# Kernel tuning notes

Hardware: AMD Instinct MI355X
Metric: run time of the kernel (lower is better)

Reference implementation:

```python
import jax, jax.numpy as jnp
import numpy as np

WS = 7        # window size
NH = 8        # num heads


def setup_inputs() -> dict:
    key = jax.random.key(0)
    ks = jax.random.split(key, 5)
    B, N, C = 32, 3136, 512
    x = jax.random.normal(ks[0], (B, N, C), dtype=jnp.float32)
    s = 1.0 / np.sqrt(C)
    w_qkv = jax.random.normal(ks[1], (C, 3 * C), dtype=jnp.float32) * s
    b_qkv = jax.random.normal(ks[2], (3 * C,), dtype=jnp.float32) * 0.01
    w_proj = jax.random.normal(ks[3], (C, C), dtype=jnp.float32) * s
    b_proj = jax.random.normal(ks[4], (C,), dtype=jnp.float32) * 0.01
    return {"x": x, "w_qkv": w_qkv, "b_qkv": b_qkv, "w_proj": w_proj, "b_proj": b_proj}


def reference(x, w_qkv, b_qkv, w_proj, b_proj):
    B, N, C = x.shape
    H = W = int(round(N ** 0.5))
    hd = C // NH
    t = WS * WS  # 49 tokens per window
    # window partition: (B,N,C) -> (nW, 49, C)
    xw = x.reshape(B, H // WS, WS, W // WS, WS, C)
    xw = jnp.transpose(xw, (0, 1, 3, 2, 4, 5)).reshape(-1, t, C)
    # qkv projection; NOTE: no head permute (faithful to source), so
    # q,k,v : (nW, 49, NH, hd)
    qkv = (xw @ w_qkv + b_qkv).reshape(-1, t, 3, NH, hd)
    q, k, v = qkv[:, :, 0], qkv[:, :, 1], qkv[:, :, 2]
    # q @ k^T contracts head_dim, attends over heads axis: (nW, 49, NH, NH)
    attn = jnp.einsum('wthd,wtgd->wthg', q, k) * (hd ** -0.5)
    attn = jax.nn.softmax(attn, axis=-1)
    out = jnp.einsum('wthg,wtgd->wthd', attn, v)          # (nW, 49, NH, hd)
    # faithful transpose(1,2).reshape(-1, 49, C) (scrambles layout, as in torch)
    out = jnp.transpose(out, (0, 2, 1, 3)).reshape(-1, t, C)
    out = out @ w_proj + b_proj
    # window merge back to (B, N, C)
    out = out.reshape(B, H // WS, W // WS, WS, WS, C)
    out = jnp.transpose(out, (0, 1, 3, 2, 4, 5)).reshape(B, N, C)
    return out
```

## Files before the change

kernel.cpp:

```cpp
#include <hip/hip_runtime.h>
#include <stdint.h>
#include <stddef.h>

typedef short s16;
typedef __attribute__((ext_vector_type(8))) short short8;
typedef __attribute__((ext_vector_type(4))) float floatx4;

__device__ __forceinline__ float bf2f(short s) {
    union { float f; uint32_t u; } c; c.u = ((uint32_t)(uint16_t)s) << 16; return c.f;
}
__device__ __forceinline__ short f2bf(float f) {
    union { float f; uint32_t u; } c; c.f = f;
    uint32_t u = c.u;
    u += 0x7fffu + ((u >> 16) & 1u);
    return (short)(u >> 16);
}

__global__ __launch_bounds__(256) void cvt_kernel(const float* __restrict__ src,
                                                  s16* __restrict__ dst) {
    size_t i = (size_t)blockIdx.x * 256 + threadIdx.x;
    const floatx4* s4 = (const floatx4*)src;
    floatx4 a = s4[i * 2], b = s4[i * 2 + 1];
    short8 o;
    o[0] = f2bf(a[0]); o[1] = f2bf(a[1]); o[2] = f2bf(a[2]); o[3] = f2bf(a[3]);
    o[4] = f2bf(b[0]); o[5] = f2bf(b[1]); o[6] = f2bf(b[2]); o[7] = f2bf(b[3]);
    ((short8*)dst)[i] = o;
}

__global__ __launch_bounds__(256) void transpose_kernel(const float* __restrict__ w,
                                                        s16* __restrict__ wt,
                                                        int K, int N) {
    int idx = blockIdx.x * 256 + threadIdx.x;
    if (idx >= K * N) return;
    int n = idx / K, k = idx - n * K;
    wt[idx] = f2bf(w[(size_t)k * N + n]);
}

__device__ __forceinline__ const s16* x_row_ptr(const s16* xb, int m) {
    int win = m / 49, t = m - win * 49;
    int b = win >> 6, rem = win & 63, hb = rem >> 3, wb = rem & 7;
    int r = t / 7, c = t - r * 7;
    int n = (hb * 7 + r) * 56 + wb * 7 + c;
    return xb + ((size_t)b * 3136 + n) * 512;
}

template <int MODE>
__global__ __launch_bounds__(512, 2) void gemm_kernel(const s16* __restrict__ A,
                                                      const s16* __restrict__ Bt,
                                                      const float* __restrict__ bias,
                                                      void* __restrict__ outp) {
    constexpr int NT  = (MODE == 0) ? 6 : 2;
    constexpr int CPX = (MODE == 0) ? 294 : 98;

    const int o  = (blockIdx.x & 7) * CPX + (blockIdx.x >> 3);
    const int tm = o / NT, tn = o - tm * NT;

    const int tid = threadIdx.x, wave = tid >> 6, lane = tid & 63;

    __shared__ s16 lA[3][256 * 32];
    __shared__ s16 lB[3][256 * 32];

    const int rloc = wave * 16 + (lane >> 2);
    const int gran = (lane & 3) * 8;
    const s16* a_src[2];
    const s16* b_src[2];
#pragma unroll
    for (int i = 0; i < 2; ++i) {
        int row = i * 128 + rloc;
        if (MODE == 0) a_src[i] = x_row_ptr(A, tm * 256 + row) + gran;
        else           a_src[i] = A + (size_t)(tm * 256 + row) * 512 + gran;
        b_src[i] = Bt + (size_t)(tn * 256 + row) * 512 + gran;
    }

#define STAGE_A(buf, i)                                                         \
    do {                                                                        \
        __builtin_amdgcn_global_load_lds(                                       \
            (const __attribute__((address_space(1))) void*)a_src[i],            \
            (__attribute__((address_space(3))) void*)&lA[buf][(i) * 4096 + wave * 512], \
            16, 0, 0);                                                          \
        a_src[i] += 32;                                                         \
    } while (0)
#define STAGE_B(buf, i)                                                         \
    do {                                                                        \
        __builtin_amdgcn_global_load_lds(                                       \
            (const __attribute__((address_space(1))) void*)b_src[i],            \
            (__attribute__((address_space(3))) void*)&lB[buf][(i) * 4096 + wave * 512], \
            16, 0, 0);                                                          \
        b_src[i] += 32;                                                         \
    } while (0)

    floatx4 acc[8][4];
#pragma unroll
    for (int mt = 0; mt < 8; ++mt)
#pragma unroll
        for (int nt = 0; nt < 4; ++nt)
            acc[mt][nt] = (floatx4){0.f, 0.f, 0.f, 0.f};

    const int wm = wave & 1, wn = wave >> 1;
    const int lm = lane & 15, quad = lane >> 4;
    const int koff = quad * 8;

    STAGE_A(0, 0); STAGE_A(0, 1); STAGE_B(0, 0); STAGE_B(0, 1);
    STAGE_A(1, 0); STAGE_A(1, 1); STAGE_B(1, 0); STAGE_B(1, 1);
    asm volatile("s_waitcnt vmcnt(4)" ::: "memory");
    __builtin_amdgcn_s_barrier();
    __builtin_amdgcn_sched_barrier(0);

#pragma unroll
    for (int kt = 0; kt < 16; ++kt) {
        const int cur = kt % 3, nxt = (kt + 2) % 3;
        short8 bq[4];
#pragma unroll
        for (int p = 0; p < 4; ++p) {
            if (p == 0) {
#pragma unroll
                for (int nt = 0; nt < 4; ++nt)
                    bq[nt] = *(const short8*)&lB[cur][(wn * 64 + nt * 16 + lm) * 32 + koff];
            }
            short8 a0 = *(const short8*)&lA[cur][(wm * 128 + (2 * p) * 16 + lm) * 32 + koff];
            short8 a1 = *(const short8*)&lA[cur][(wm * 128 + (2 * p + 1) * 16 + lm) * 32 + koff];

            if (kt < 14) {
                if      (p == 0) STAGE_A(nxt, 0);
                else if (p == 1) STAGE_A(nxt, 1);
                else if (p == 2) STAGE_B(nxt, 0);
                else             STAGE_B(nxt, 1);
            }

            __builtin_amdgcn_s_barrier();
            asm volatile("s_waitcnt lgkmcnt(0)" ::: "memory");
            __builtin_amdgcn_sched_barrier(0);

            __builtin_amdgcn_s_setprio(1);
#pragma unroll
            for (int nt = 0; nt < 4; ++nt)
                acc[2 * p][nt] = __builtin_amdgcn_mfma_f32_16x16x32_bf16(
                    a0, bq[nt], acc[2 * p][nt], 0, 0, 0);
#pragma unroll
            for (int nt = 0; nt < 4; ++nt)
                acc[2 * p + 1][nt] = __builtin_amdgcn_mfma_f32_16x16x32_bf16(
                    a1, bq[nt], acc[2 * p + 1][nt], 0, 0, 0);
            __builtin_amdgcn_s_setprio(0);

            if (p == 3) {
                if (kt < 14)       asm volatile("s_waitcnt vmcnt(4)" ::: "memory");
                else if (kt == 14) asm volatile("s_waitcnt vmcnt(0)" ::: "memory");
            }
            if (!(kt == 15 && p == 3)) {
                __builtin_amdgcn_s_barrier();
                __builtin_amdgcn_sched_barrier(0);
            }
        }
    }
#undef STAGE_A
#undef STAGE_B

    float bv[4];
#pragma unroll
    for (int nt = 0; nt < 4; ++nt)
        bv[nt] = bias[tn * 256 + wn * 64 + nt * 16 + lm];

#pragma unroll
    for (int mt = 0; mt < 8; ++mt) {
        int mbase = tm * 256 + wm * 128 + mt * 16 + quad * 4;
#pragma unroll
        for (int i = 0; i < 4; ++i) {
            int m = mbase + i;
            size_t rowoff;
            if (MODE == 1) {
                int win = m / 49, t = m - win * 49;
                int b = win >> 6, rem = win & 63, hb = rem >> 3, wb = rem & 7;
                int r = t / 7, c = t - r * 7;
                int n = (hb * 7 + r) * 56 + wb * 7 + c;
                rowoff = ((size_t)b * 3136 + n) * 512;
            } else {
                rowoff = (size_t)m * 1536;
            }
#pragma unroll
            for (int nt = 0; nt < 4; ++nt) {
                int coln = tn * 256 + wn * 64 + nt * 16 + lm;
                float v = acc[mt][nt][i] + bv[nt];
                if (MODE == 0) ((s16*)outp)[rowoff + coln] = f2bf(v);
                else           ((float*)outp)[rowoff + coln] = v;
            }
        }
    }
}

__global__ __launch_bounds__(256) void attn_kernel(const s16* __restrict__ qkv,
                                                   s16* __restrict__ attn) {
    const int tid = threadIdx.x, wave = tid >> 6, lane = tid & 63;
    const int m = blockIdx.x * 4 + wave;

    __shared__ s16 sh[4][1536];
    s16* my = sh[wave];
    const s16* row = qkv + (size_t)m * 1536;
#pragma unroll
    for (int i = 0; i < 3; ++i)
        *(short8*)&my[i * 512 + lane * 8] = *(const short8*)&row[i * 512 + lane * 8];
    __syncthreads();

    const int h = lane >> 3, g = lane & 7;
    const s16* qs = my + h * 64;
    const s16* ks = my + 512 + g * 64;
    const s16* vs = my + 1024;

    float s = 0.f;
#pragma unroll
    for (int db = 0; db < 8; ++db) {
        int d0 = ((db + h) & 7) * 8;
        short8 q8 = *(const short8*)&qs[d0];
        short8 k8 = *(const short8*)&ks[d0];
#pragma unroll
        for (int j = 0; j < 8; ++j) s += bf2f(q8[j]) * bf2f(k8[j]);
    }
    s *= 0.125f;

    float mx = s;
    mx = fmaxf(mx, __shfl_xor(mx, 1));
    mx = fmaxf(mx, __shfl_xor(mx, 2));
    mx = fmaxf(mx, __shfl_xor(mx, 4));
    float p = __expf(s - mx);
    float sum = p;
    sum += __shfl_xor(sum, 1);
    sum += __shfl_xor(sum, 2);
    sum += __shfl_xor(sum, 4);
    p /= sum;

    float o[8];
#pragma unroll
    for (int j = 0; j < 8; ++j) o[j] = 0.f;
    const int dgrp = (lane & 7) * 8;
#pragma unroll
    for (int gg = 0; gg < 8; ++gg) {
        float pg = __shfl(p, h * 8 + gg);
        short8 v8 = *(const short8*)&vs[gg * 64 + dgrp];
#pragma unroll
        for (int j = 0; j < 8; ++j) o[j] += pg * bf2f(v8[j]);
    }

    int win = m / 49, t = m - win * 49;
    s16* dst = attn + (size_t)win * 25088 + h * 3136 + t * 64 + dgrp;
    short8 ob;
#pragma unroll
    for (int j = 0; j < 8; ++j) ob[j] = f2bf(o[j]);
    *(short8*)dst = ob;
}

extern "C" void kernel_launch(void* const* d_in, const int* in_sizes, int n_in,
                              void* d_out, int out_size, void* d_ws, size_t ws_size,
                              hipStream_t stream) {
    const float* x      = (const float*)d_in[0];
    const float* w_qkv  = (const float*)d_in[1];
    const float* b_qkv  = (const float*)d_in[2];
    const float* w_proj = (const float*)d_in[3];
    const float* b_proj = (const float*)d_in[4];

    char* ws = (char*)d_ws;
    s16* xbf    = (s16*)ws;
    s16* qkv    = (s16*)(ws + 102760448ull);
    s16* attn   = (s16*)(ws + 102760448ull + 308281344ull);
    s16* wqkvT  = (s16*)(ws + 102760448ull + 308281344ull + 102760448ull);
    s16* wprojT = (s16*)(ws + 102760448ull + 308281344ull + 102760448ull + 1572864ull);

    cvt_kernel<<<25088, 256, 0, stream>>>(x, xbf);
    transpose_kernel<<<3072, 256, 0, stream>>>(w_qkv, wqkvT, 512, 1536);
    transpose_kernel<<<1024, 256, 0, stream>>>(w_proj, wprojT, 512, 512);
    gemm_kernel<0><<<392 * 6, 512, 0, stream>>>(xbf, wqkvT, b_qkv, qkv);
    attn_kernel<<<25088, 256, 0, stream>>>(qkv, attn);
    gemm_kernel<1><<<392 * 2, 512, 0, stream>>>(attn, wprojT, b_proj, d_out);
}
```

Before: 759.9 us.

## Swizzle LDS k-granules and restructure GEMM k-loop into two MFMA phases

XOR-swizzles the 16-byte k-granule position per row when staging A/B into LDS and when reading fragments, to reduce LDS bank conflicts on the short8 reads. The inner k-tile loop is reorganised from four sub-phases with a barrier pair each into two phases of 16 MFMAs, loading all B and half of A fragments up front. This cuts barrier count per k-tile and batches MFMAs, at the cost of more live fragment registers and coarser interleaving of global-to-LDS staging.

After: 714.1 us. 1.06x faster.

```diff
diff --git a/kernel.cpp b/kernel.cpp
--- a/kernel.cpp
+++ b/kernel.cpp
@@ -61,7 +61,7 @@
     __shared__ s16 lB[3][256 * 32];
 
     const int rloc = wave * 16 + (lane >> 2);
-    const int gran = (lane & 3) * 8;
+    const int gran = (((lane & 3) ^ ((lane >> 3) & 3)) << 3);
     const s16* a_src[2];
     const s16* b_src[2];
 #pragma unroll
@@ -98,7 +98,7 @@
 
     const int wm = wave & 1, wn = wave >> 1;
     const int lm = lane & 15, quad = lane >> 4;
-    const int koff = quad * 8;
+    const int swz = ((quad ^ ((lm >> 1) & 3)) << 3);
 
     STAGE_A(0, 0); STAGE_A(0, 1); STAGE_B(0, 0); STAGE_B(0, 1);
     STAGE_A(1, 0); STAGE_A(1, 1); STAGE_B(1, 0); STAGE_B(1, 1);
@@ -109,47 +109,55 @@
 #pragma unroll
     for (int kt = 0; kt < 16; ++kt) {
         const int cur = kt % 3, nxt = (kt + 2) % 3;
-        short8 bq[4];
-#pragma unroll
-        for (int p = 0; p < 4; ++p) {
-            if (p == 0) {
-#pragma unroll
-                for (int nt = 0; nt < 4; ++nt)
-                    bq[nt] = *(const short8*)&lB[cur][(wn * 64 + nt * 16 + lm) * 32 + koff];
-            }
-            short8 a0 = *(const short8*)&lA[cur][(wm * 128 + (2 * p) * 16 + lm) * 32 + koff];
-            short8 a1 = *(const short8*)&lA[cur][(wm * 128 + (2 * p + 1) * 16 + lm) * 32 + koff];
-
-            if (kt < 14) {
-                if      (p == 0) STAGE_A(nxt, 0);
-                else if (p == 1) STAGE_A(nxt, 1);
-                else if (p == 2) STAGE_B(nxt, 0);
-                else             STAGE_B(nxt, 1);
-            }
-
+
+        short8 bq[4], af[4];
+#pragma unroll
+        for (int nt = 0; nt < 4; ++nt)
+            bq[nt] = *(const short8*)&lB[cur][(wn * 64 + nt * 16 + lm) * 32 + swz];
+#pragma unroll
+        for (int mt = 0; mt < 4; ++mt)
+            af[mt] = *(const short8*)&lA[cur][(wm * 128 + mt * 16 + lm) * 32 + swz];
+        if (kt < 14) { STAGE_A(nxt, 0); STAGE_A(nxt, 1); }
+
+        __builtin_amdgcn_s_barrier();
+        asm volatile("s_waitcnt lgkmcnt(0)" ::: "memory");
+        __builtin_amdgcn_sched_barrier(0);
+
+        __builtin_amdgcn_s_setprio(1);
+#pragma unroll
+        for (int mt = 0; mt < 4; ++mt)
+#pragma unroll
+            for (int nt = 0; nt < 4; ++nt)
+                acc[mt][nt] = __builtin_amdgcn_mfma_f32_16x16x32_bf16(
+                    af[mt], bq[nt], acc[mt][nt], 0, 0, 0);
+        __builtin_amdgcn_s_setprio(0);
+        __builtin_amdgcn_s_barrier();
+        __builtin_amdgcn_sched_barrier(0);
+
+        short8 ag[4];
+#pragma unroll
+        for (int mt = 0; mt < 4; ++mt)
+            ag[mt] = *(const short8*)&lA[cur][(wm * 128 + (mt + 4) * 16 + lm) * 32 + swz];
+        if (kt < 14) { STAGE_B(nxt, 0); STAGE_B(nxt, 1); }
+
+        __builtin_amdgcn_s_barrier();
+        asm volatile("s_waitcnt lgkmcnt(0)" ::: "memory");
+        __builtin_amdgcn_sched_barrier(0);
+
+        __builtin_amdgcn_s_setprio(1);
+#pragma unroll
+        for (int mt = 0; mt < 4; ++mt)
+#pragma unroll
+            for (int nt = 0; nt < 4; ++nt)
+                acc[mt + 4][nt] = __builtin_amdgcn_mfma_f32_16x16x32_bf16(
+                    ag[mt], bq[nt], acc[mt + 4][nt], 0, 0, 0);
+        __builtin_amdgcn_s_setprio(0);
+
+        if (kt < 14)       asm volatile("s_waitcnt vmcnt(4)" ::: "memory");
+        else if (kt == 14) asm volatile("s_waitcnt vmcnt(0)" ::: "memory");
+        if (kt != 15) {
             __builtin_amdgcn_s_barrier();
-            asm volatile("s_waitcnt lgkmcnt(0)" ::: "memory");
             __builtin_amdgcn_sched_barrier(0);
-
-            __builtin_amdgcn_s_setprio(1);
-#pragma unroll
-            for (int nt = 0; nt < 4; ++nt)
-                acc[2 * p][nt] = __builtin_amdgcn_mfma_f32_16x16x32_bf16(
-                    a0, bq[nt], acc[2 * p][nt], 0, 0, 0);
-#pragma unroll
-            for (int nt = 0; nt < 4; ++nt)
-                acc[2 * p + 1][nt] = __builtin_amdgcn_mfma_f32_16x16x32_bf16(
-                    a1, bq[nt], acc[2 * p + 1][nt], 0, 0, 0);
-            __builtin_amdgcn_s_setprio(0);
-
-            if (p == 3) {
-                if (kt < 14)       asm volatile("s_waitcnt vmcnt(4)" ::: "memory");
-                else if (kt == 14) asm volatile("s_waitcnt vmcnt(0)" ::: "memory");
-            }
-            if (!(kt == 15 && p == 3)) {
-                __builtin_amdgcn_s_barrier();
-                __builtin_amdgcn_sched_barrier(0);
-            }
         }
     }
 #undef STAGE_A
```
